# Kernel tuning notes

Measured on AMD Instinct MI355X. Metric: run time of the kernel, lower is better.

Reference implementation:

```python
import jax, jax.numpy as jnp
import numpy as np

F_FIELDS = 39
VOCAB = 200000
EMB = 16
D1 = 32
BATCH = 16384


def setup_inputs() -> dict:
    key = jax.random.key(0)
    ks = jax.random.split(key, 12)
    Xi = jax.random.randint(ks[0], (BATCH, F_FIELDS, 1), 0, VOCAB, dtype=jnp.int64 if jax.config.jax_enable_x64 else jnp.int32)
    Xv = jax.random.uniform(ks[1], (BATCH, F_FIELDS), dtype=jnp.float32)
    # one table per field, all same vocab -> stacked [F, V, E]
    tables = jax.random.normal(ks[2], (F_FIELDS, VOCAB, EMB), dtype=jnp.float32) * 0.05
    W1 = jax.random.normal(ks[3], (D1, F_FIELDS, EMB), dtype=jnp.float32)   # first_order_weight
    Wi = jax.random.normal(ks[4], (D1, F_FIELDS, EMB), dtype=jnp.float32)   # inner_second_weight_emb
    lin1_w = jax.random.normal(ks[5], (32, 32), dtype=jnp.float32) * (1.0 / np.sqrt(32))
    lin1_b = jax.random.normal(ks[6], (32,), dtype=jnp.float32) * 0.01
    lin2_w = jax.random.normal(ks[7], (32, 32), dtype=jnp.float32) * (1.0 / np.sqrt(32))
    lin2_b = jax.random.normal(ks[8], (32,), dtype=jnp.float32) * 0.01
    last_w = jax.random.normal(ks[9], (1, 32), dtype=jnp.float32) * (1.0 / np.sqrt(32))
    last_b = jax.random.normal(ks[10], (1,), dtype=jnp.float32) * 0.01
    return {"Xi": Xi, "Xv": Xv, "tables": tables, "W1": W1, "Wi": Wi,
            "lin1_w": lin1_w, "lin1_b": lin1_b, "lin2_w": lin2_w, "lin2_b": lin2_b,
            "last_w": last_w, "last_b": last_b}


def reference(Xi, Xv, tables, W1, Wi, lin1_w, lin1_b, lin2_w, lin2_b, last_w, last_b):
    # Per-field embedding lookup; Xi[:, f, 0] indexes field f's table.
    idx = Xi[:, :, 0]                                   # [B, F]
    emb = tables[jnp.arange(F_FIELDS)[None, :], idx]    # [B, F, E]
    emb = emb * Xv[:, :, None]                          # scale by feature value
    # first-order product layer: sum_j <emb_j, w_{i,j}> for each output unit i
    first_order = jnp.einsum('bfe,dfe->bd', emb, W1)    # [B, D1]
    # inner-product term: (sum_j <emb_j, wi_{i,j}>)^2
    s = jnp.einsum('bfe,dfe->bd', emb, Wi)
    x = first_order + s * s                             # [B, D1]
    # deep MLP (relu, eval mode: no dropout; bias param in original is unused in forward)
    x = jax.nn.relu(x @ lin1_w.T + lin1_b)
    x = jax.nn.relu(x @ lin2_w.T + lin2_b)
    out = x @ last_w.T + last_b                         # [B, 1]
    return jnp.sum(out, axis=1)                         # [B]
```

## Files before the change

### kernel.cpp

```cpp
#include <hip/hip_runtime.h>
#include <stdint.h>
#include <stddef.h>

#define F_FIELDS 39
#define VOCAB    200000
#define EMB      16
#define BATCH    16384
#define MBLK     32
#define NOUT     64
#define KPAD     640
#define NCHUNK   10
#define KC       64
#define ASTR     88
#define BSTR     88
#define CSTR     68

typedef __attribute__((ext_vector_type(8))) short bf16x8;
typedef __attribute__((ext_vector_type(4))) float f32x4;

__device__ __forceinline__ unsigned short f2bf(float x) {
  union { float f; unsigned int u; } a; a.f = x;
  unsigned int r = (a.u + 0x7fffu + ((a.u >> 16) & 1u)) >> 16;
  return (unsigned short)r;
}
__device__ __forceinline__ float bf2f(unsigned short h) {
  union { unsigned int u; float f; } a; a.u = ((unsigned int)h) << 16;
  return a.f;
}

__global__ void prep_w(const float* __restrict__ W1, const float* __restrict__ Wi,
                       unsigned short* __restrict__ Wt) {
  int i = blockIdx.x * 256 + threadIdx.x;
  if (i >= NOUT * KPAD) return;
  int n = i / KPAD, k = i % KPAD;
  float v = 0.0f;
  if (k < F_FIELDS * EMB) v = (n < 32) ? W1[n * 624 + k] : Wi[(n - 32) * 624 + k];
  Wt[i] = f2bf(v);
}

__global__ __launch_bounds__(256) void pnn_main(
    const int* __restrict__ Xi, const float* __restrict__ Xv,
    const float* __restrict__ tables, const unsigned short* __restrict__ Wt,
    const float* __restrict__ lin1_w, const float* __restrict__ lin1_b,
    const float* __restrict__ lin2_w, const float* __restrict__ lin2_b,
    const float* __restrict__ last_w, const float* __restrict__ last_b,
    float* __restrict__ out)
{
  const int t    = threadIdx.x;
  const int wave = t >> 6, lane = t & 63;
  const int l15  = lane & 15, quad = lane >> 4;

  __shared__ unsigned short A_sh[MBLK * ASTR];
  __shared__ unsigned short Al_sh[MBLK * ASTR];
  __shared__ unsigned short B_sh[NOUT * BSTR];
  __shared__ float          C_sh[MBLK * CSTR];
  __shared__ float          X1_sh[MBLK * 36];
  __shared__ float          W_lds[2145];

  for (int i = t; i < 1024; i += 256) {
    W_lds[i]        = lin1_w[i];
    W_lds[1024 + i] = lin2_w[i];
  }
  if (t < 32) {
    W_lds[2048 + t] = lin1_b[t];
    W_lds[2080 + t] = lin2_b[t];
    W_lds[2112 + t] = last_w[t];
  }
  if (t == 0) W_lds[2144] = last_b[0];

  const int gm    = t & 31;
  const int gfl   = (t >> 5) & 3;
  const int ghalf = t >> 7;
  const int sample = blockIdx.x * MBLK + gm;

  int   idxs[NCHUNK];
  float xvs[NCHUNK];
#pragma unroll
  for (int c = 0; c < NCHUNK; ++c) {
    int f = c * 4 + gfl;
    bool v = (f < F_FIELDS);
    int g = sample * F_FIELDS + (v ? f : 0);
    idxs[c] = v ? Xi[g] : 0;
    xvs[c]  = v ? Xv[g] : 0.0f;
  }

  const int bn = t >> 2, bseg = t & 3;

  const int m_tile = wave & 1, n_half = wave >> 1;
  const int arow = m_tile * 16 + l15;
  const int nb0  = n_half * 32 + l15;

  f32x4 acc0 = {0.f, 0.f, 0.f, 0.f};
  f32x4 acc1 = {0.f, 0.f, 0.f, 0.f};

#pragma unroll
  for (int c = 0; c < NCHUNK; ++c) {
    {
      const uint4* src = (const uint4*)(Wt + bn * KPAD + c * KC + bseg * 16);
      uint4 w0 = src[0], w1 = src[1];
      uint4* dst = (uint4*)&B_sh[bn * BSTR + bseg * 16];
      dst[0] = w0; dst[1] = w1;
    }
    {
      int f = c * 4 + gfl;
      float4 v0 = {0.f,0.f,0.f,0.f}, v1 = {0.f,0.f,0.f,0.f};
      float xv = xvs[c];
      if (f < F_FIELDS) {
        const float* p = tables + ((size_t)f * VOCAB + (size_t)idxs[c]) * EMB + ghalf * 8;
        v0 = *(const float4*)p;
        v1 = *(const float4*)(p + 4);
      }
      float vals[8] = { v0.x * xv, v0.y * xv, v0.z * xv, v0.w * xv,
                        v1.x * xv, v1.y * xv, v1.z * xv, v1.w * xv };
      union { unsigned short us[8]; uint4 v; } hi, lo;
#pragma unroll
      for (int j = 0; j < 8; ++j) {
        unsigned short h = f2bf(vals[j]);
        hi.us[j] = h;
        lo.us[j] = f2bf(vals[j] - bf2f(h));
      }
      *(uint4*)&A_sh[gm * ASTR + gfl * 16 + ghalf * 8]  = hi.v;
      *(uint4*)&Al_sh[gm * ASTR + gfl * 16 + ghalf * 8] = lo.v;
    }
    __syncthreads();
#pragma unroll
    for (int kk = 0; kk < 2; ++kk) {
      bf16x8 ah = *(const bf16x8*)&A_sh[arow * ASTR + kk * 32 + quad * 8];
      bf16x8 al = *(const bf16x8*)&Al_sh[arow * ASTR + kk * 32 + quad * 8];
      bf16x8 b0 = *(const bf16x8*)&B_sh[nb0 * BSTR + kk * 32 + quad * 8];
      bf16x8 b1 = *(const bf16x8*)&B_sh[(nb0 + 16) * BSTR + kk * 32 + quad * 8];
      acc0 = __builtin_amdgcn_mfma_f32_16x16x32_bf16(ah, b0, acc0, 0, 0, 0);
      acc1 = __builtin_amdgcn_mfma_f32_16x16x32_bf16(ah, b1, acc1, 0, 0, 0);
      acc0 = __builtin_amdgcn_mfma_f32_16x16x32_bf16(al, b0, acc0, 0, 0, 0);
      acc1 = __builtin_amdgcn_mfma_f32_16x16x32_bf16(al, b1, acc1, 0, 0, 0);
    }
    __syncthreads();
  }

  {
    int row_base = m_tile * 16 + quad * 4;
    int col0 = n_half * 32 + l15;
#pragma unroll
    for (int r = 0; r < 4; ++r) {
      C_sh[(row_base + r) * CSTR + col0]      = acc0[r];
      C_sh[(row_base + r) * CSTR + col0 + 16] = acc1[r];
    }
  }
  __syncthreads();

  {
    int m = t >> 3, j0 = (t & 7) * 4;
#pragma unroll
    for (int j = 0; j < 4; ++j) {
      float fo = C_sh[m * CSTR + j0 + j];
      float s  = C_sh[m * CSTR + 32 + j0 + j];
      C_sh[m * CSTR + j0 + j] = fo + s * s;
    }
  }
  __syncthreads();

  {
    const int m = t >> 3, d0 = (t & 7) * 4;
    float a0 = W_lds[2048 + d0 + 0];
    float a1 = W_lds[2048 + d0 + 1];
    float a2 = W_lds[2048 + d0 + 2];
    float a3 = W_lds[2048 + d0 + 3];
#pragma unroll
    for (int j = 0; j < 32; ++j) {
      float xj = C_sh[m * CSTR + j];
      a0 = fmaf(W_lds[(d0 + 0) * 32 + j], xj, a0);
      a1 = fmaf(W_lds[(d0 + 1) * 32 + j], xj, a1);
      a2 = fmaf(W_lds[(d0 + 2) * 32 + j], xj, a2);
      a3 = fmaf(W_lds[(d0 + 3) * 32 + j], xj, a3);
    }
    X1_sh[m * 36 + d0 + 0] = fmaxf(a0, 0.0f);
    X1_sh[m * 36 + d0 + 1] = fmaxf(a1, 0.0f);
    X1_sh[m * 36 + d0 + 2] = fmaxf(a2, 0.0f);
    X1_sh[m * 36 + d0 + 3] = fmaxf(a3, 0.0f);
  }
  __syncthreads();

  {
    const int m = t >> 3, d0 = (t & 7) * 4;
    float a0 = W_lds[2080 + d0 + 0];
    float a1 = W_lds[2080 + d0 + 1];
    float a2 = W_lds[2080 + d0 + 2];
    float a3 = W_lds[2080 + d0 + 3];
#pragma unroll
    for (int j = 0; j < 32; ++j) {
      float xj = X1_sh[m * 36 + j];
      a0 = fmaf(W_lds[1024 + (d0 + 0) * 32 + j], xj, a0);
      a1 = fmaf(W_lds[1024 + (d0 + 1) * 32 + j], xj, a1);
      a2 = fmaf(W_lds[1024 + (d0 + 2) * 32 + j], xj, a2);
      a3 = fmaf(W_lds[1024 + (d0 + 3) * 32 + j], xj, a3);
    }
    C_sh[m * CSTR + 32 + d0 + 0] = fmaxf(a0, 0.0f);
    C_sh[m * CSTR + 32 + d0 + 1] = fmaxf(a1, 0.0f);
    C_sh[m * CSTR + 32 + d0 + 2] = fmaxf(a2, 0.0f);
    C_sh[m * CSTR + 32 + d0 + 3] = fmaxf(a3, 0.0f);
  }
  __syncthreads();

  if (t < MBLK) {
    float s = W_lds[2144];
#pragma unroll
    for (int j = 0; j < 32; ++j)
      s = fmaf(W_lds[2112 + j], C_sh[t * CSTR + 32 + j], s);
    out[blockIdx.x * MBLK + t] = s;
  }
}

extern "C" void kernel_launch(void* const* d_in, const int* in_sizes, int n_in,
                              void* d_out, int out_size, void* d_ws, size_t ws_size,
                              hipStream_t stream) {
  (void)in_sizes; (void)n_in; (void)out_size; (void)ws_size;
  const int*   Xi     = (const int*)d_in[0];
  const float* Xv     = (const float*)d_in[1];
  const float* tables = (const float*)d_in[2];
  const float* W1     = (const float*)d_in[3];
  const float* Wi     = (const float*)d_in[4];
  const float* l1w    = (const float*)d_in[5];
  const float* l1b    = (const float*)d_in[6];
  const float* l2w    = (const float*)d_in[7];
  const float* l2b    = (const float*)d_in[8];
  const float* lw     = (const float*)d_in[9];
  const float* lb     = (const float*)d_in[10];
  float* out = (float*)d_out;

  unsigned short* Wt = (unsigned short*)d_ws;

  prep_w<<<dim3((NOUT * KPAD + 255) / 256), dim3(256), 0, stream>>>(W1, Wi, Wt);
  pnn_main<<<dim3(BATCH / MBLK), dim3(256), 0, stream>>>(
      Xi, Xv, tables, Wt, l1w, l1b, l2w, l2b, lw, lb, out);
}
```

Before: 577.8 us.

## Load embedding and weight fragments directly into MFMA registers with prefetching

```diff
diff --git a/kernel.cpp b/kernel.cpp
--- a/kernel.cpp
+++ b/kernel.cpp
@@ -6,13 +6,10 @@
 #define VOCAB    200000
 #define EMB      16
 #define BATCH    16384
-#define MBLK     32
+#define MBLK     64
 #define NOUT     64
 #define KPAD     640
 #define NCHUNK   10
-#define KC       64
-#define ASTR     88
-#define BSTR     88
 #define CSTR     68
 
 typedef __attribute__((ext_vector_type(8))) short bf16x8;
@@ -22,10 +19,6 @@
   union { float f; unsigned int u; } a; a.f = x;
   unsigned int r = (a.u + 0x7fffu + ((a.u >> 16) & 1u)) >> 16;
   return (unsigned short)r;
-}
-__device__ __forceinline__ float bf2f(unsigned short h) {
-  union { unsigned int u; float f; } a; a.u = ((unsigned int)h) << 16;
-  return a.f;
 }
 
 __global__ void prep_w(const float* __restrict__ W1, const float* __restrict__ Wi,
@@ -35,10 +28,56 @@
   int n = i / KPAD, k = i % KPAD;
   float v = 0.0f;
   if (k < F_FIELDS * EMB) v = (n < 32) ? W1[n * 624 + k] : Wi[(n - 32) * 624 + k];
-  Wt[i] = f2bf(v);
-}
-
-__global__ __launch_bounds__(256) void pnn_main(
+  Wt[(k >> 3) * 512 + n * 8 + (k & 7)] = f2bf(v);
+}
+
+
+#define PNN_ISSUE_A(c) do {                                                   \
+  _Pragma("unroll")                                                           \
+  for (int h_ = 0; h_ < 2; ++h_) {                                           \
+    int f_ = (c) * 4 + h_ * 2 + q2;                                          \
+    if (f_ >= F_FIELDS) f_ = 0;           \
+    const float* p_ = tb + (unsigned)((f_ * VOCAB + idxv[(c)][h_]) * EMB);   \
+    va[(c) % 3][h_][0] = *(const float4*)p_;                                 \
+    va[(c) % 3][h_][1] = *(const float4*)(p_ + 4);                           \
+  }                                                                           \
+} while (0)
+
+#define PNN_ISSUE_B(c) do {                                                   \
+  _Pragma("unroll")                                                           \
+  for (int kk_ = 0; kk_ < 2; ++kk_) {                                        \
+    const unsigned short* pc_ = pB + ((c) * 2 + kk_) * 2048;                 \
+    vb[(c) % 2][kk_][0] = *(const bf16x8*)pc_;                               \
+    vb[(c) % 2][kk_][1] = *(const bf16x8*)(pc_ + 128);                       \
+  }                                                                           \
+} while (0)
+
+#define PNN_COMPUTE(c) do {                                                   \
+  _Pragma("unroll")                                                           \
+  for (int kk_ = 0; kk_ < 2; ++kk_) {                                        \
+    const float xv_ = xvv[(c)][kk_];                                         \
+    const float4 v0_ = va[(c) % 3][kk_][0];                                  \
+    const float4 v1_ = va[(c) % 3][kk_][1];                                  \
+    const float vals_[8] = { v0_.x * xv_, v0_.y * xv_, v0_.z * xv_, v0_.w * xv_, \
+                             v1_.x * xv_, v1_.y * xv_, v1_.z * xv_, v1_.w * xv_ }; \
+    bf16x8 ah_, al_;                                                          \
+    _Pragma("unroll")                                                         \
+    for (int j_ = 0; j_ < 8; ++j_) {                                         \
+      union { float f; unsigned int u; } a_; a_.f = vals_[j_];               \
+      union { unsigned int u; float f; } b_; b_.u = a_.u & 0xffff0000u;      \
+      ah_[j_] = (short)(a_.u >> 16);                                         \
+      al_[j_] = (short)f2bf(vals_[j_] - b_.f);                               \
+    }                                                                         \
+    const bf16x8 b0_ = vb[(c) % 2][kk_][0];                                  \
+    const bf16x8 b1_ = vb[(c) % 2][kk_][1];                                  \
+    acc0 = __builtin_amdgcn_mfma_f32_16x16x32_bf16(ah_, b0_, acc0, 0, 0, 0); \
+    acc1 = __builtin_amdgcn_mfma_f32_16x16x32_bf16(ah_, b1_, acc1, 0, 0, 0); \
+    acc0 = __builtin_amdgcn_mfma_f32_16x16x32_bf16(al_, b0_, acc0, 0, 0, 0); \
+    acc1 = __builtin_amdgcn_mfma_f32_16x16x32_bf16(al_, b1_, acc1, 0, 0, 0); \
+  }                                                                           \
+} while (0)
+
+__global__ __launch_bounds__(512, 2) void pnn_main(
     const int* __restrict__ Xi, const float* __restrict__ Xv,
     const float* __restrict__ tables, const unsigned short* __restrict__ Wt,
     const float* __restrict__ lin1_w, const float* __restrict__ lin1_b,
@@ -49,15 +88,14 @@
   const int t    = threadIdx.x;
   const int wave = t >> 6, lane = t & 63;
   const int l15  = lane & 15, quad = lane >> 4;
-
-  __shared__ unsigned short A_sh[MBLK * ASTR];
-  __shared__ unsigned short Al_sh[MBLK * ASTR];
-  __shared__ unsigned short B_sh[NOUT * BSTR];
-  __shared__ float          C_sh[MBLK * CSTR];
-  __shared__ float          X1_sh[MBLK * 36];
-  __shared__ float          W_lds[2145];
-
-  for (int i = t; i < 1024; i += 256) {
+  const int q2   = quad >> 1, qh = quad & 1;
+  const int m_tile = wave & 3, n_half = wave >> 2;
+
+  __shared__ float C_sh[MBLK * CSTR];
+  __shared__ float X1_sh[MBLK * 36];
+  __shared__ float W_lds[2145];
+
+  for (int i = t; i < 1024; i += 512) {
     W_lds[i]        = lin1_w[i];
     W_lds[1024 + i] = lin2_w[i];
   }
@@ -68,73 +106,38 @@
   }
   if (t == 0) W_lds[2144] = last_b[0];
 
-  const int gm    = t & 31;
-  const int gfl   = (t >> 5) & 3;
-  const int ghalf = t >> 7;
-  const int sample = blockIdx.x * MBLK + gm;
-
-  int   idxs[NCHUNK];
-  float xvs[NCHUNK];
+  const int sample = blockIdx.x * MBLK + m_tile * 16 + l15;
+
+  int   idxv[NCHUNK][2];
+  float xvv[NCHUNK][2];
 #pragma unroll
   for (int c = 0; c < NCHUNK; ++c) {
-    int f = c * 4 + gfl;
-    bool v = (f < F_FIELDS);
-    int g = sample * F_FIELDS + (v ? f : 0);
-    idxs[c] = v ? Xi[g] : 0;
-    xvs[c]  = v ? Xv[g] : 0.0f;
-  }
-
-  const int bn = t >> 2, bseg = t & 3;
-
-  const int m_tile = wave & 1, n_half = wave >> 1;
-  const int arow = m_tile * 16 + l15;
-  const int nb0  = n_half * 32 + l15;
-
+#pragma unroll
+    for (int h = 0; h < 2; ++h) {
+      int f = c * 4 + h * 2 + q2;
+      bool valid = (f < F_FIELDS);
+      int g = sample * F_FIELDS + (valid ? f : 0);
+      idxv[c][h] = valid ? Xi[g] : 0;
+      xvv[c][h]  = valid ? Xv[g] : 0.0f;
+    }
+  }
+
+  const float* tb = tables + qh * 8;
+  const unsigned short* pB = Wt + quad * 512 + (n_half * 32 + l15) * 8;
+
+  float4 va[3][2][2];
+  bf16x8 vb[2][2][2];
   f32x4 acc0 = {0.f, 0.f, 0.f, 0.f};
   f32x4 acc1 = {0.f, 0.f, 0.f, 0.f};
 
+  PNN_ISSUE_A(0);
+  PNN_ISSUE_A(1);
+  PNN_ISSUE_B(0);
 #pragma unroll
   for (int c = 0; c < NCHUNK; ++c) {
-    {
-      const uint4* src = (const uint4*)(Wt + bn * KPAD + c * KC + bseg * 16);
-      uint4 w0 = src[0], w1 = src[1];
-      uint4* dst = (uint4*)&B_sh[bn * BSTR + bseg * 16];
-      dst[0] = w0; dst[1] = w1;
-    }
-    {
-      int f = c * 4 + gfl;
-      float4 v0 = {0.f,0.f,0.f,0.f}, v1 = {0.f,0.f,0.f,0.f};
-      float xv = xvs[c];
-      if (f < F_FIELDS) {
-        const float* p = tables + ((size_t)f * VOCAB + (size_t)idxs[c]) * EMB + ghalf * 8;
-        v0 = *(const float4*)p;
-        v1 = *(const float4*)(p + 4);
-      }
-      float vals[8] = { v0.x * xv, v0.y * xv, v0.z * xv, v0.w * xv,
-                        v1.x * xv, v1.y * xv, v1.z * xv, v1.w * xv };
-      union { unsigned short us[8]; uint4 v; } hi, lo;
-#pragma unroll
-      for (int j = 0; j < 8; ++j) {
-        unsigned short h = f2bf(vals[j]);
-        hi.us[j] = h;
-        lo.us[j] = f2bf(vals[j] - bf2f(h));
-      }
-      *(uint4*)&A_sh[gm * ASTR + gfl * 16 + ghalf * 8]  = hi.v;
-      *(uint4*)&Al_sh[gm * ASTR + gfl * 16 + ghalf * 8] = lo.v;
-    }
-    __syncthreads();
-#pragma unroll
-    for (int kk = 0; kk < 2; ++kk) {
-      bf16x8 ah = *(const bf16x8*)&A_sh[arow * ASTR + kk * 32 + quad * 8];
-      bf16x8 al = *(const bf16x8*)&Al_sh[arow * ASTR + kk * 32 + quad * 8];
-      bf16x8 b0 = *(const bf16x8*)&B_sh[nb0 * BSTR + kk * 32 + quad * 8];
-      bf16x8 b1 = *(const bf16x8*)&B_sh[(nb0 + 16) * BSTR + kk * 32 + quad * 8];
-      acc0 = __builtin_amdgcn_mfma_f32_16x16x32_bf16(ah, b0, acc0, 0, 0, 0);
-      acc1 = __builtin_amdgcn_mfma_f32_16x16x32_bf16(ah, b1, acc1, 0, 0, 0);
-      acc0 = __builtin_amdgcn_mfma_f32_16x16x32_bf16(al, b0, acc0, 0, 0, 0);
-      acc1 = __builtin_amdgcn_mfma_f32_16x16x32_bf16(al, b1, acc1, 0, 0, 0);
-    }
-    __syncthreads();
+    if (c + 2 < NCHUNK) PNN_ISSUE_A(c + 2);
+    if (c + 1 < NCHUNK) PNN_ISSUE_B(c + 1);
+    PNN_COMPUTE(c);
   }
 
   {
@@ -230,6 +233,6 @@
   unsigned short* Wt = (unsigned short*)d_ws;
 
   prep_w<<<dim3((NOUT * KPAD + 255) / 256), dim3(256), 0, stream>>>(W1, Wi, Wt);
-  pnn_main<<<dim3(BATCH / MBLK), dim3(256), 0, stream>>>(
+  pnn_main<<<dim3(BATCH / MBLK), dim3(512), 0, stream>>>(
       Xi, Xv, tables, Wt, l1w, l1b, l2w, l2b, lw, lb, out);
 }
```

Measured after the change: 583.7 us. Within noise of the previous version (+1.0%).
